# Kernel tuning notes

Hardware: AMD Instinct MI355X
Metric: run time of the kernel (lower is better)

Reference implementation:

```python
import jax, jax.numpy as jnp
import numpy as np

B, L, HID = 2, 2048, 2048
NH, NKV, HD = 16, 4, 128
LAT = 512
Q_PER_KV = NH // NKV
SCALE = HD ** -0.5
ROPE_THETA = 10000.0


def setup_inputs() -> dict:
    key = jax.random.key(0)
    ks = jax.random.split(key, 6)
    s = lambda fan_in: 1.0 / np.sqrt(fan_in)
    return {
        "x": jax.random.normal(ks[0], (B, L, HID), dtype=jnp.float32),
        "Wq": jax.random.normal(ks[1], (HID, NH * HD), dtype=jnp.float32) * s(HID),
        "Wc": jax.random.normal(ks[2], (HID, LAT), dtype=jnp.float32) * s(HID),
        "Wk": jax.random.normal(ks[3], (LAT, NKV * HD), dtype=jnp.float32) * s(LAT),
        "Wv": jax.random.normal(ks[4], (LAT, NKV * HD), dtype=jnp.float32) * s(LAT),
        "Wo": jax.random.normal(ks[5], (NH * HD, HID), dtype=jnp.float32) * s(NH * HD),
        "attention_mask": jnp.ones((B, L), dtype=jnp.int32),
    }


def _rope(t):  # t: [B, H, L, HD]
    half = HD // 2
    inv_freq = 1.0 / (ROPE_THETA ** (jnp.arange(half, dtype=jnp.float32) / half))
    pos = jnp.arange(t.shape[2], dtype=jnp.float32)
    freqs = pos[:, None] * inv_freq[None, :]          # [L, half]
    cos = jnp.cos(freqs)[None, None].astype(t.dtype)  # [1,1,L,half]
    sin = jnp.sin(freqs)[None, None].astype(t.dtype)
    t1, t2 = t[..., :half], t[..., half:]
    return jnp.concatenate([t1 * cos - t2 * sin, t2 * cos + t1 * sin], axis=-1)


def reference(x, Wq, Wc, Wk, Wv, Wo, attention_mask):
    q = (x @ Wq).reshape(B, L, NH, HD).transpose(0, 2, 1, 3)      # [B,NH,L,HD]
    c = x @ Wc                                                    # latent bottleneck
    k = (c @ Wk).reshape(B, L, NKV, HD).transpose(0, 2, 1, 3)     # [B,NKV,L,HD]
    v = (c @ Wv).reshape(B, L, NKV, HD).transpose(0, 2, 1, 3)
    # GQA repeat_interleave along head axis
    k = jnp.repeat(k, Q_PER_KV, axis=1)                           # [B,NH,L,HD]
    v = jnp.repeat(v, Q_PER_KV, axis=1)
    q = _rope(q)
    k = _rope(k)
    att = jnp.einsum("bhqd,bhkd->bhqk", q, k) * SCALE             # [B,NH,L,L]
    neg = jnp.finfo(att.dtype).min
    causal = jnp.tril(jnp.ones((L, L), dtype=bool))[None, None]
    att = jnp.where(causal, att, neg)
    key_mask = (attention_mask > 0)[:, None, None, :]             # [B,1,1,L]
    att = jnp.where(key_mask, att, neg)
    att = jax.nn.softmax(att, axis=-1)
    y = jnp.einsum("bhqk,bhkd->bhqd", att, v)
    y = y.transpose(0, 2, 1, 3).reshape(B, L, NH * HD)
    return y @ Wo
```

## Files before the change

### kernel.cpp

```cpp
#include <hip/hip_runtime.h>
#include <hip/hip_bf16.h>
#include <cstdint>
#include <cstddef>

#define B_    2
#define L_    2048
#define HID_  2048
#define NH_   16
#define NKV_  4
#define HD_   128
#define LAT_  512
#define SCALE_ 0.08838834764831845f
#define SC2_   0.1275174365f

typedef unsigned short u16;
typedef unsigned int   u32;
typedef __attribute__((ext_vector_type(8))) short   short8;
typedef __attribute__((ext_vector_type(4))) float   floatx4;

typedef __attribute__((address_space(1))) const u32 gas_u32;
typedef __attribute__((address_space(3))) u32       las_u32;

__device__ __forceinline__ void gl_lds16(const u16* g, u16* l) {
    __builtin_amdgcn_global_load_lds((gas_u32*)g, (las_u32*)l, 16, 0, 0);
}

__device__ __forceinline__ float bf2f(u16 u) {
    union { u32 i; float f; } v; v.i = ((u32)u) << 16; return v.f;
}
__device__ __forceinline__ u16 f2bf(float f) {
    union { float f; u32 u; } v; v.f = f;
    u32 u = v.u;
    u32 r = (u + 0x7fffu + ((u >> 16) & 1u)) >> 16;
    return (u16)r;
}
__device__ __forceinline__ u16 f2bf_hw(float f) {
    union { __hip_bfloat16 h; u16 u; } c;
    c.h = __float2bfloat16(f);
    return c.u;
}

__global__ void cvt_kernel(const float* __restrict__ in, u16* __restrict__ out, int n4) {
    int i = blockIdx.x * 256 + threadIdx.x;
    if (i < n4) {
        float4 v = ((const float4*)in)[i];
        union { u16 w[4]; uint2 v; } o;
        o.w[0] = f2bf(v.x); o.w[1] = f2bf(v.y);
        o.w[2] = f2bf(v.z); o.w[3] = f2bf(v.w);
        ((uint2*)out)[i] = o.v;
    }
}

__global__ void cvt_transpose2_kernel(const float* __restrict__ in0, u16* __restrict__ out0,
                                      const float* __restrict__ in1, u16* __restrict__ out1,
                                      int R, int C) {
    __shared__ u16 tile[32][33];
    const float* in = blockIdx.z ? in1 : in0;
    u16* out = blockIdx.z ? out1 : out0;
    int c0 = blockIdx.x * 32, r0 = blockIdx.y * 32;
    int tx = threadIdx.x & 31, ty = threadIdx.x >> 5;
    for (int i = ty; i < 32; i += 8)
        tile[tx][i] = f2bf(in[(size_t)(r0 + i) * C + c0 + tx]);
    __syncthreads();
    for (int i = ty; i < 32; i += 8)
        out[(size_t)(c0 + i) * R + r0 + tx] = tile[i][tx];
}

__global__ void transpose_v_kernel(const u16* __restrict__ kv, u16* __restrict__ out) {
    __shared__ u16 t[32][33];
    int lt = blockIdx.x, dt = blockIdx.y, bh = blockIdx.z;
    int b = bh >> 2, kvh = bh & 3;
    int tx = threadIdx.x & 31, ty = threadIdx.x >> 5;
    for (int i = ty; i < 32; i += 8)
        t[i][tx] = kv[(size_t)(b * L_ + lt * 32 + i) * 1024 + 512 + kvh * HD_ + dt * 32 + tx];
    __syncthreads();
    const int lcol = lt * 32 + tx;
    const int k6 = lcol & 63;
    const int ni = k6 >> 4, qd = (k6 >> 2) & 3, r = k6 & 3;
    const int p = ((ni >> 1) << 5) | (qd << 3) | ((ni & 1) << 2) | r;
    const int csig = (lcol & ~63) | p;
    for (int i = ty; i < 32; i += 8)
        out[((size_t)bh * HD_ + dt * 32 + i) * L_ + csig] = t[tx][i];
}

template<int OUT_BF16>
__global__ __launch_bounds__(256)
void gemm_bt(const u16* __restrict__ A, const u16* __restrict__ BT,
             void* __restrict__ C, int M, int N, int K) {
    __shared__ __align__(16) u16 As[128][64];
    __shared__ __align__(16) u16 Bs[128][64];
    const int tid  = threadIdx.x;
    const int m0   = blockIdx.y * 128, n0 = blockIdx.x * 128;
    const int wave = tid >> 6, lane = tid & 63;
    const int wm   = (wave >> 1) * 64, wn = (wave & 1) * 64;
    const int quad = lane >> 4, l16 = lane & 15;

    const int r8 = lane >> 3, srcc = ((lane & 7) ^ r8) * 8;
    const int row0 = wave * 32 + r8;
    const u16* aBase = A  + (size_t)(m0 + row0) * K + srcc;
    const u16* bBase = BT + (size_t)(n0 + row0) * K + srcc;
    u16* laBase = &As[0][0] + wave * 2048;
    u16* lbBase = &Bs[0][0] + wave * 2048;

    floatx4 acc[4][4] = {};

    for (int k0 = 0; k0 < K; k0 += 64) {
        #pragma unroll
        for (int cc = 0; cc < 4; ++cc) {
            gl_lds16(aBase + (size_t)cc * 8 * K + k0, laBase + cc * 512);
            gl_lds16(bBase + (size_t)cc * 8 * K + k0, lbBase + cc * 512);
        }
        __syncthreads();

        #pragma unroll
        for (int kk = 0; kk < 2; kk++) {
            short8 af[4], bfr[4];
            const int co = ((kk * 4 + quad) ^ (l16 & 7)) * 8;
            #pragma unroll
            for (int i = 0; i < 4; i++) {
                af[i]  = *(const short8*)&As[wm + i * 16 + l16][co];
                bfr[i] = *(const short8*)&Bs[wn + i * 16 + l16][co];
            }
            #pragma unroll
            for (int mi = 0; mi < 4; mi++)
                #pragma unroll
                for (int ni = 0; ni < 4; ni++)
                    acc[mi][ni] = __builtin_amdgcn_mfma_f32_16x16x32_bf16(
                        af[mi], bfr[ni], acc[mi][ni], 0, 0, 0);
        }
        __syncthreads();
    }

    #pragma unroll
    for (int mi = 0; mi < 4; mi++) {
        #pragma unroll
        for (int ni = 0; ni < 4; ni++) {
            #pragma unroll
            for (int r = 0; r < 4; r++) {
                int row = m0 + wm + mi * 16 + quad * 4 + r;
                int col = n0 + wn + ni * 16 + l16;
                float v = acc[mi][ni][r];
                if (OUT_BF16) ((u16*)C)[(size_t)row * N + col] = f2bf(v);
                else          ((float*)C)[(size_t)row * N + col] = v;
            }
        }
    }
}

__global__ __launch_bounds__(256)
void gemm_bt_split(const u16* __restrict__ A, const u16* __restrict__ BT,
                   u16* __restrict__ C0, u16* __restrict__ C1,
                   int M, int N, int K, int Nsplit, int N0, int N1) {
    __shared__ __align__(16) u16 As[128][64];
    __shared__ __align__(16) u16 Bs[128][64];
    const int tid  = threadIdx.x;
    const int m0   = blockIdx.y * 128, n0 = blockIdx.x * 128;
    const int wave = tid >> 6, lane = tid & 63;
    const int wm   = (wave >> 1) * 64, wn = (wave & 1) * 64;
    const int quad = lane >> 4, l16 = lane & 15;

    const int r8 = lane >> 3, srcc = ((lane & 7) ^ r8) * 8;
    const int row0 = wave * 32 + r8;
    const u16* aBase = A  + (size_t)(m0 + row0) * K + srcc;
    const u16* bBase = BT + (size_t)(n0 + row0) * K + srcc;
    u16* laBase = &As[0][0] + wave * 2048;
    u16* lbBase = &Bs[0][0] + wave * 2048;

    floatx4 acc[4][4] = {};

    for (int k0 = 0; k0 < K; k0 += 64) {
        #pragma unroll
        for (int cc = 0; cc < 4; ++cc) {
            gl_lds16(aBase + (size_t)cc * 8 * K + k0, laBase + cc * 512);
            gl_lds16(bBase + (size_t)cc * 8 * K + k0, lbBase + cc * 512);
        }
        __syncthreads();

        #pragma unroll
        for (int kk = 0; kk < 2; kk++) {
            short8 af[4], bfr[4];
            const int co = ((kk * 4 + quad) ^ (l16 & 7)) * 8;
            #pragma unroll
            for (int i = 0; i < 4; i++) {
                af[i]  = *(const short8*)&As[wm + i * 16 + l16][co];
                bfr[i] = *(const short8*)&Bs[wn + i * 16 + l16][co];
            }
            #pragma unroll
            for (int mi = 0; mi < 4; mi++)
                #pragma unroll
                for (int ni = 0; ni < 4; ni++)
                    acc[mi][ni] = __builtin_amdgcn_mfma_f32_16x16x32_bf16(
                        af[mi], bfr[ni], acc[mi][ni], 0, 0, 0);
        }
        __syncthreads();
    }

    const int side = (n0 >= Nsplit);
    u16* Cw = side ? C1 : C0;
    const int nw = side ? N1 : N0;
    const int cbase = side ? Nsplit : 0;

    #pragma unroll
    for (int mi = 0; mi < 4; mi++) {
        #pragma unroll
        for (int ni = 0; ni < 4; ni++) {
            #pragma unroll
            for (int r = 0; r < 4; r++) {
                int row = m0 + wm + mi * 16 + quad * 4 + r;
                int col = n0 + wn + ni * 16 + l16 - cbase;
                Cw[(size_t)row * nw + col] = f2bf(acc[mi][ni][r]);
            }
        }
    }
}

__global__ void rope_perm(const u16* __restrict__ in, u16* __restrict__ out,
                          int nh, int nhbits, int rs) {
    int idx = blockIdx.x * 256 + threadIdx.x;
    int d = idx & 63;
    int l = (idx >> 6) & (L_ - 1);
    int h = (idx >> 17) & (nh - 1);
    int b = idx >> (17 + nhbits);
    const u16* src = &in[(size_t)(b * L_ + l) * rs + h * HD_];
    u16* dst = &out[(((size_t)b * nh + h) * L_ + l) * HD_];
    float t1 = bf2f(src[d]), t2 = bf2f(src[d + 64]);
    float inv = expf(-(float)d * 0.14391156831212787f);
    float fr = (float)l * inv;
    float c = cosf(fr), sn = sinf(fr);
    dst[d]      = f2bf(t1 * c - t2 * sn);
    dst[d + 64] = f2bf(t2 * c + t1 * sn);
}

__global__ __launch_bounds__(256)
void attn_mfma(const u16* __restrict__ Q, const u16* __restrict__ K,
               const u16* __restrict__ Vt, const int* __restrict__ amask,
               u16* __restrict__ Y, float* __restrict__ Opart,
               float* __restrict__ lpart) {
    __shared__ __align__(16) u16 Ks[2][64][128];
    __shared__ __align__(16) u16 Vs[2][128][64];

    const int tid  = threadIdx.x;
    const int wave = tid >> 6, lane = tid & 63;
    const int quad = lane >> 4, l16 = lane & 15;

    const int bid = blockIdx.x;
    const int s   = bid >> 8;
    const int c   = bid & 255;
    const int bkvh = c & 7;
    const int j   = c >> 3;
    const int b   = bkvh >> 2, kvh = bkvh & 3;

    const int H  = ((32 + j) >> 1) + 1;
    const int Lg = ((31 - j) >> 1) + 1;
    const int m2 = max((H + 1) >> 1, (Lg + 1) >> 1);
    const int m3 = max((H + 2) / 3, Lg);
    const int nh = (m2 <= m3) ? 2 : 3;
    const int nl = 4 - nh;
    int t, kt0, kt1, pi;
    if (s < nh) {
        t = 32 + j; kt0 = (H * s) / nh; kt1 = (H * (s + 1)) / nh; pi = bid;
    } else {
        t = 31 - j;
        const int ls = s - nh;
        kt0 = (Lg * ls) / nl; kt1 = (Lg * (ls + 1)) / nl;
        pi = (nl == 1) ? -1 : bid;
    }

    const int h   = kvh * 4 + wave;
    const int q0  = t * 32;

    const u16* Qbase = Q  + ((size_t)b * NH_  + h)   * L_ * HD_;
    const u16* Kbase = K  + ((size_t)b * NKV_ + kvh) * L_ * HD_;
    const u16* Vbase = Vt + ((size_t)b * NKV_ + kvh) * (size_t)HD_ * L_;
    const int* mbase = amask + b * L_;

    short8 qa[2][4];
    #pragma unroll
    for (int mi = 0; mi < 2; ++mi)
        #pragma unroll
        for (int ks = 0; ks < 4; ++ks)
            qa[mi][ks] = *(const short8*)&Qbase[(size_t)(q0 + mi * 16 + l16) * HD_ + ks * 32 + quad * 8];

    floatx4 Oacc[2][8] = {};
    float lsum[2] = {0.0f, 0.0f};

    const int slK = lane & 15, rKl = lane >> 4;
    const int slV = lane & 7,  rVl = lane >> 3;
    int okg[4], ovg[4];
    u16 *klds[4], *vlds[4];
    #pragma unroll
    for (int cc = 0; cc < 4; ++cc) {
        const int seg = wave * 4 + cc;
        const int rk = seg * 4 + rKl;
        okg[cc] = rk * HD_ + ((slK ^ (rk & 7)) * 8);
        klds[cc] = &Ks[0][0][0] + seg * 512;
        const int rv = seg * 8 + rVl;
        ovg[cc] = rv * L_ + ((slV ^ (rv & 7)) * 8);
        vlds[cc] = &Vs[0][0][0] + seg * 512;
    }
    const u16* kgb = Kbase + (size_t)kt0 * 64 * HD_;
    const u16* vgb = Vbase + kt0 * 64;

    #pragma unroll
    for (int cc = 0; cc < 4; ++cc) {
        gl_lds16(kgb + okg[cc], klds[cc]);
        gl_lds16(vgb + ovg[cc], vlds[cc]);
    }
    kgb += (size_t)64 * HD_;
    vgb += 64;

    int bufoff = 0;
    for (int kt = kt0; kt < kt1; ++kt) {
        const int kbase = kt * 64;

        __syncthreads();

        const int nb = bufoff ^ 8192;
        if (kt + 1 < kt1) {
            #pragma unroll
            for (int cc = 0; cc < 4; ++cc) {
                gl_lds16(kgb + okg[cc], klds[cc] + nb);
                gl_lds16(vgb + ovg[cc], vlds[cc] + nb);
            }
            kgb += (size_t)64 * HD_;
            vgb += 64;
        }
        const int am_l = mbase[kbase + lane];
        const bool allm = __all(am_l > 0);
        const u16* KsB = &Ks[0][0][0] + bufoff;
        const u16* VsB = &Vs[0][0][0] + bufoff;

        floatx4 sfr[2][4] = {};
        __builtin_amdgcn_s_setprio(1);
        #pragma unroll
        for (int ni = 0; ni < 4; ++ni) {
            #pragma unroll
            for (int ks = 0; ks < 4; ++ks) {
                short8 kf = *(const short8*)&KsB[(ni * 16 + l16) * 128 + ((ks * 4 + quad) ^ (l16 & 7)) * 8];
                sfr[0][ni] = __builtin_amdgcn_mfma_f32_16x16x32_bf16(kf, qa[0][ks], sfr[0][ni], 0, 0, 0);
                sfr[1][ni] = __builtin_amdgcn_mfma_f32_16x16x32_bf16(kf, qa[1][ks], sfr[1][ni], 0, 0, 0);
            }
        }
        __builtin_amdgcn_s_setprio(0);

        if (allm & (kbase + 63 <= q0)) {
            #pragma unroll
            for (int mi = 0; mi < 2; ++mi)
                #pragma unroll
                for (int ni = 0; ni < 4; ++ni)
                    #pragma unroll
                    for (int r = 0; r < 4; ++r) {
                        float p = exp2f(fmaf(sfr[mi][ni][r], SC2_, -8.0f));
                        lsum[mi] += p;
                        sfr[mi][ni][r] = p;
                    }
        } else {
            #pragma unroll
            for (int ni = 0; ni < 4; ++ni) {
                const int4 amv = *(const int4*)&mbase[kbase + ni * 16 + quad * 4];
                const int amr[4] = {amv.x, amv.y, amv.z, amv.w};
                #pragma unroll
                for (int mi = 0; mi < 2; ++mi) {
                    const int qrow = q0 + mi * 16 + l16;
                    #pragma unroll
                    for (int r = 0; r < 4; ++r) {
                        const int kpos = kbase + ni * 16 + quad * 4 + r;
                        const bool ok = (kpos <= qrow) & (amr[r] > 0);
                        float p = ok ? exp2f(fmaf(sfr[mi][ni][r], SC2_, -8.0f)) : 0.0f;
                        lsum[mi] += p;
                        sfr[mi][ni][r] = p;
                    }
                }
            }
        }

        short8 pf[2][2];
        #pragma unroll
        for (int mi = 0; mi < 2; ++mi)
            #pragma unroll
            for (int kc = 0; kc < 2; ++kc) {
                union { u16 w[8]; short8 s8; } u;
                #pragma unroll
                for (int r = 0; r < 4; ++r) {
                    u.w[r]     = f2bf_hw(sfr[mi][kc * 2][r]);
                    u.w[4 + r] = f2bf_hw(sfr[mi][kc * 2 + 1][r]);
                }
                pf[mi][kc] = u.s8;
            }

        __builtin_amdgcn_s_setprio(1);
        #pragma unroll
        for (int kc = 0; kc < 2; ++kc) {
            #pragma unroll
            for (int dn = 0; dn < 8; ++dn) {
                short8 vf = *(const short8*)&VsB[(dn * 16 + l16) * 64 + ((kc * 4 + quad) ^ (l16 & 7)) * 8];
                Oacc[0][dn] = __builtin_amdgcn_mfma_f32_16x16x32_bf16(pf[0][kc], vf, Oacc[0][dn], 0, 0, 0);
                Oacc[1][dn] = __builtin_amdgcn_mfma_f32_16x16x32_bf16(pf[1][kc], vf, Oacc[1][dn], 0, 0, 0);
            }
        }
        __builtin_amdgcn_s_setprio(0);

        bufoff = nb;
    }

    float lr[2];
    #pragma unroll
    for (int mi = 0; mi < 2; ++mi) {
        float v = lsum[mi];
        v += __shfl_xor(v, 16);
        v += __shfl_xor(v, 32);
        lr[mi] = v;
    }

    if (pi < 0) {
        #pragma unroll
        for (int mi = 0; mi < 2; ++mi) {
            #pragma unroll
            for (int r = 0; r < 4; ++r) {
                const float linv = 1.0f / __shfl(lr[mi], quad * 4 + r);
                const int qrow = q0 + mi * 16 + quad * 4 + r;
                u16* dst = &Y[(((size_t)b * L_ + qrow) * NH_ + h) * HD_];
                #pragma unroll
                for (int dn = 0; dn < 8; ++dn)
                    dst[dn * 16 + l16] = f2bf(Oacc[mi][dn][r] * linv);
            }
        }
    } else {
        float* od = Opart + ((size_t)pi * 4 + wave) * 32 * 128;
        float* lp = lpart + ((size_t)pi * 4 + wave) * 32;
        #pragma unroll
        for (int mi = 0; mi < 2; ++mi) {
            if (quad == 0)
                __builtin_nontemporal_store(lr[mi], &lp[mi * 16 + l16]);
            #pragma unroll
            for (int r = 0; r < 4; ++r) {
                const int qi = mi * 16 + quad * 4 + r;
                #pragma unroll
                for (int dn = 0; dn < 8; ++dn)
                    __builtin_nontemporal_store(Oacc[mi][dn][r],
                                                &od[(size_t)qi * 128 + dn * 16 + l16]);
            }
        }
    }
}

__global__ __launch_bounds__(256)
void attn_combine(const float* __restrict__ Opart, const float* __restrict__ lpart,
                  u16* __restrict__ Y) {
    const int cb = blockIdx.x;
    const int c  = cb & 255, z = cb >> 8;
    const int tile = z >> 2, hw = z & 3;
    const int bkvh = c & 7, j = c >> 3;
    const int b = bkvh >> 2, kvh = bkvh & 3;
    const int h = kvh * 4 + hw;
    const int H  = ((32 + j) >> 1) + 1;
    const int Lg = ((31 - j) >> 1) + 1;
    const int m2 = max((H + 1) >> 1, (Lg + 1) >> 1);
    const int m3 = max((H + 2) / 3, Lg);
    const int nh = (m2 <= m3) ? 2 : 3;
    const int nl = 4 - nh;
    if (tile == 1 && nl == 1) return;
    const int s0 = tile ? nh : 0;
    const int ns = tile ? nl : nh;
    const int t  = tile ? (31 - j) : (32 + j);
    const int tid = threadIdx.x;
    const int q = tid >> 3, dg = tid & 7;

    float4 a0 = {0,0,0,0}, a1 = {0,0,0,0}, a2 = {0,0,0,0}, a3 = {0,0,0,0};
    float lacc = 0.0f;
    for (int i = 0; i < ns; ++i) {
        const size_t rowb = ((size_t)((s0 + i) * 256 + c) * 4 + hw) * 32 + q;
        lacc += lpart[rowb];
        const float4* op = (const float4*)(Opart + rowb * 128 + dg * 16);
        float4 v0 = op[0], v1 = op[1], v2 = op[2], v3 = op[3];
        a0.x += v0.x; a0.y += v0.y; a0.z += v0.z; a0.w += v0.w;
        a1.x += v1.x; a1.y += v1.y; a1.z += v1.z; a1.w += v1.w;
        a2.x += v2.x; a2.y += v2.y; a2.z += v2.z; a2.w += v2.w;
        a3.x += v3.x; a3.y += v3.y; a3.z += v3.z; a3.w += v3.w;
    }
    const float linv = 1.0f / lacc;
    const int qrow = t * 32 + q;
    u16* dst = &Y[(((size_t)b * L_ + qrow) * NH_ + h) * HD_ + dg * 16];

    u16 tmp[16];
    tmp[0]  = f2bf(a0.x * linv); tmp[1]  = f2bf(a0.y * linv);
    tmp[2]  = f2bf(a0.z * linv); tmp[3]  = f2bf(a0.w * linv);
    tmp[4]  = f2bf(a1.x * linv); tmp[5]  = f2bf(a1.y * linv);
    tmp[6]  = f2bf(a1.z * linv); tmp[7]  = f2bf(a1.w * linv);
    tmp[8]  = f2bf(a2.x * linv); tmp[9]  = f2bf(a2.y * linv);
    tmp[10] = f2bf(a2.z * linv); tmp[11] = f2bf(a2.w * linv);
    tmp[12] = f2bf(a3.x * linv); tmp[13] = f2bf(a3.y * linv);
    tmp[14] = f2bf(a3.z * linv); tmp[15] = f2bf(a3.w * linv);
    *(uint4*)(dst)     = *(const uint4*)(&tmp[0]);
    *(uint4*)(dst + 8) = *(const uint4*)(&tmp[8]);
}

extern "C" void kernel_launch(void* const* d_in, const int* in_sizes, int n_in,
                              void* d_out, int out_size, void* d_ws, size_t ws_size,
                              hipStream_t stream) {
    const float* x  = (const float*)d_in[0];
    const float* Wq = (const float*)d_in[1];
    const float* Wc = (const float*)d_in[2];
    const float* Wk = (const float*)d_in[3];
    const float* Wv = (const float*)d_in[4];
    const float* Wo = (const float*)d_in[5];
    const int* amask = (const int*)d_in[6];
    float* out = (float*)d_out;

    char* p = (char*)d_ws;
    auto alloc = [&](size_t elems) {
        u16* r = (u16*)p;
        p += ((elems * 2 + 255) / 256) * 256;
        return r;
    };
    u16* WoT  = alloc((size_t)2048 * 2048);
    u16* qbuf = alloc((size_t)4096 * 2048);
    u16* Qr   = alloc((size_t)4096 * 2048);
    u16* Kr   = alloc((size_t)4096 * 512);
    u16* Vt   = alloc((size_t)4096 * 512);
    char* pdead = p;
    u16* WqT  = alloc((size_t)2048 * 2048);
    u16* WckvT= alloc((size_t)1024 * 2048);
    u16* WkT  = alloc((size_t)512 * 512);
    u16* WvT  = alloc((size_t)512 * 512);
    u16* Wcb  = alloc((size_t)2048 * 512);
    u16* Xb   = alloc((size_t)4096 * 2048);
    u16* kvbuf= alloc((size_t)4096 * 1024);
    float* Opart = (float*)pdead;
    float* lpart = (float*)(pdead + (size_t)1024 * 4 * 32 * 128 * 4);

    cvt_kernel<<<8388608 / 4 / 256, 256, 0, stream>>>(x, Xb, 8388608 / 4);
    cvt_kernel<<<(2048 * 512 / 4) / 256, 256, 0, stream>>>(Wc, Wcb, 2048 * 512 / 4);
    cvt_transpose2_kernel<<<dim3(64, 64, 2), 256, 0, stream>>>(Wq, WqT, Wo, WoT, 2048, 2048);
    cvt_transpose2_kernel<<<dim3(16, 16, 2), 256, 0, stream>>>(Wk, WkT, Wv, WvT, 512, 512);

    gemm_bt<1><<<dim3(16, 8), 256, 0, stream>>>(WkT, Wcb, WckvT, 1024, 2048, 512);

    gemm_bt_split<<<dim3(24, 32), 256, 0, stream>>>(Xb, WqT, qbuf, kvbuf,
                                                    4096, 3072, 2048, 2048, 2048, 1024);

    rope_perm<<<(2 * 16 * 2048 * 64) / 256, 256, 0, stream>>>(qbuf, Qr, 16, 4, 2048);
    rope_perm<<<(2 * 4 * 2048 * 64) / 256, 256, 0, stream>>>(kvbuf, Kr, 4, 2, 1024);
    transpose_v_kernel<<<dim3(64, 4, 8), 256, 0, stream>>>(kvbuf, Vt);

    attn_mfma<<<dim3(1024), 256, 0, stream>>>(Qr, Kr, Vt, amask, qbuf, Opart, lpart);
    attn_combine<<<dim3(2048), 256, 0, stream>>>(Opart, lpart, qbuf);

    gemm_bt<0><<<dim3(16, 32), 256, 0, stream>>>(qbuf, WoT, out, 4096, 2048, 2048);
}
```

Measured before the change: 339.3 us.

## Rebalance attention work split and fuse small prep kernel launches

The attention kernel drops from 1024 blocks to 512. Each block either handles the first 17 key tiles of a high query tile, or the rest of that tile followed by the whole paired low query tile, in two sequential passes. The combine step now only merges high-tile partials, and the Opart buffer shrinks. Rope for Q and K and the V transpose are merged into a single launch, as are the two fp32-to-bf16 conversions, to cut launch overhead. Halving the grid lowers parallelism and lengthens per-block serial work, so CU occupancy on a 256-CU part may drop.

Measured after the change: 324.6 us. -4.3%, faster.

```diff
diff --git a/kernel.cpp b/kernel.cpp
--- a/kernel.cpp
+++ b/kernel.cpp
@@ -40,15 +40,18 @@
     return c.u;
 }
 
-__global__ void cvt_kernel(const float* __restrict__ in, u16* __restrict__ out, int n4) {
+__global__ void cvt2_kernel(const float* __restrict__ in0, u16* __restrict__ out0, int n40,
+                            const float* __restrict__ in1, u16* __restrict__ out1, int n41) {
     int i = blockIdx.x * 256 + threadIdx.x;
-    if (i < n4) {
-        float4 v = ((const float4*)in)[i];
-        union { u16 w[4]; uint2 v; } o;
-        o.w[0] = f2bf(v.x); o.w[1] = f2bf(v.y);
-        o.w[2] = f2bf(v.z); o.w[3] = f2bf(v.w);
-        ((uint2*)out)[i] = o.v;
-    }
+    const float* in; u16* out; int k;
+    if (i < n40) { in = in0; out = out0; k = i; }
+    else if (i < n40 + n41) { in = in1; out = out1; k = i - n40; }
+    else return;
+    float4 v = ((const float4*)in)[k];
+    union { u16 w[4]; uint2 v; } o;
+    o.w[0] = f2bf(v.x); o.w[1] = f2bf(v.y);
+    o.w[2] = f2bf(v.z); o.w[3] = f2bf(v.w);
+    ((uint2*)out)[k] = o.v;
 }
 
 __global__ void cvt_transpose2_kernel(const float* __restrict__ in0, u16* __restrict__ out0,
@@ -66,21 +69,47 @@
         out[(size_t)(c0 + i) * R + r0 + tx] = tile[i][tx];
 }
 
-__global__ void transpose_v_kernel(const u16* __restrict__ kv, u16* __restrict__ out) {
-    __shared__ u16 t[32][33];
-    int lt = blockIdx.x, dt = blockIdx.y, bh = blockIdx.z;
-    int b = bh >> 2, kvh = bh & 3;
-    int tx = threadIdx.x & 31, ty = threadIdx.x >> 5;
-    for (int i = ty; i < 32; i += 8)
-        t[i][tx] = kv[(size_t)(b * L_ + lt * 32 + i) * 1024 + 512 + kvh * HD_ + dt * 32 + tx];
-    __syncthreads();
-    const int lcol = lt * 32 + tx;
-    const int k6 = lcol & 63;
-    const int ni = k6 >> 4, qd = (k6 >> 2) & 3, r = k6 & 3;
-    const int p = ((ni >> 1) << 5) | (qd << 3) | ((ni & 1) << 2) | r;
-    const int csig = (lcol & ~63) | p;
-    for (int i = ty; i < 32; i += 8)
-        out[((size_t)bh * HD_ + dt * 32 + i) * L_ + csig] = t[tx][i];
+#define NRQ_ 16384
+#define NRK_ 4096
+__global__ void prep_qkv(const u16* __restrict__ qbuf, u16* __restrict__ Qr,
+                         const u16* __restrict__ kvbuf, u16* __restrict__ Kr,
+                         u16* __restrict__ Vt) {
+    __shared__ u16 tvt[32][33];
+    const int bb = blockIdx.x;
+    if (bb < NRQ_ + NRK_) {
+        const bool isq = bb < NRQ_;
+        const u16* in = isq ? qbuf : kvbuf;
+        u16* out = isq ? Qr : Kr;
+        const int nh = isq ? 16 : 4, nhbits = isq ? 4 : 2, rs = isq ? 2048 : 1024;
+        int idx = (isq ? bb : bb - NRQ_) * 256 + threadIdx.x;
+        int d = idx & 63;
+        int l = (idx >> 6) & (L_ - 1);
+        int h = (idx >> 17) & (nh - 1);
+        int b = idx >> (17 + nhbits);
+        const u16* src = &in[(size_t)(b * L_ + l) * rs + h * HD_];
+        u16* dst = &out[(((size_t)b * nh + h) * L_ + l) * HD_];
+        float t1 = bf2f(src[d]), t2 = bf2f(src[d + 64]);
+        float inv = expf(-(float)d * 0.14391156831212787f);
+        float fr = (float)l * inv;
+        float c = cosf(fr), sn = sinf(fr);
+        dst[d]      = f2bf(t1 * c - t2 * sn);
+        dst[d + 64] = f2bf(t2 * c + t1 * sn);
+    } else {
+        const int i = bb - NRQ_ - NRK_;
+        const int lt = i & 63, dt = (i >> 6) & 3, bh = i >> 8;
+        const int b = bh >> 2, kvh = bh & 3;
+        const int tx = threadIdx.x & 31, ty = threadIdx.x >> 5;
+        for (int k = ty; k < 32; k += 8)
+            tvt[k][tx] = kvbuf[(size_t)(b * L_ + lt * 32 + k) * 1024 + 512 + kvh * HD_ + dt * 32 + tx];
+        __syncthreads();
+        const int lcol = lt * 32 + tx;
+        const int k6 = lcol & 63;
+        const int ni = k6 >> 4, qd = (k6 >> 2) & 3, r = k6 & 3;
+        const int p = ((ni >> 1) << 5) | (qd << 3) | ((ni & 1) << 2) | r;
+        const int csig = (lcol & ~63) | p;
+        for (int k = ty; k < 32; k += 8)
+            Vt[((size_t)bh * HD_ + dt * 32 + k) * L_ + csig] = tvt[tx][k];
+    }
 }
 
 template<int OUT_BF16>
@@ -214,23 +243,6 @@
     }
 }
 
-__global__ void rope_perm(const u16* __restrict__ in, u16* __restrict__ out,
-                          int nh, int nhbits, int rs) {
-    int idx = blockIdx.x * 256 + threadIdx.x;
-    int d = idx & 63;
-    int l = (idx >> 6) & (L_ - 1);
-    int h = (idx >> 17) & (nh - 1);
-    int b = idx >> (17 + nhbits);
-    const u16* src = &in[(size_t)(b * L_ + l) * rs + h * HD_];
-    u16* dst = &out[(((size_t)b * nh + h) * L_ + l) * HD_];
-    float t1 = bf2f(src[d]), t2 = bf2f(src[d + 64]);
-    float inv = expf(-(float)d * 0.14391156831212787f);
-    float fr = (float)l * inv;
-    float c = cosf(fr), sn = sinf(fr);
-    dst[d]      = f2bf(t1 * c - t2 * sn);
-    dst[d + 64] = f2bf(t2 * c + t1 * sn);
-}
-
 __global__ __launch_bounds__(256)
 void attn_mfma(const u16* __restrict__ Q, const u16* __restrict__ K,
                const u16* __restrict__ Vt, const int* __restrict__ amask,
@@ -251,38 +263,13 @@
     const int b   = bkvh >> 2, kvh = bkvh & 3;
 
     const int H  = ((32 + j) >> 1) + 1;
-    const int Lg = ((31 - j) >> 1) + 1;
-    const int m2 = max((H + 1) >> 1, (Lg + 1) >> 1);
-    const int m3 = max((H + 2) / 3, Lg);
-    const int nh = (m2 <= m3) ? 2 : 3;
-    const int nl = 4 - nh;
-    int t, kt0, kt1, pi;
-    if (s < nh) {
-        t = 32 + j; kt0 = (H * s) / nh; kt1 = (H * (s + 1)) / nh; pi = bid;
-    } else {
-        t = 31 - j;
-        const int ls = s - nh;
-        kt0 = (Lg * ls) / nl; kt1 = (Lg * (ls + 1)) / nl;
-        pi = (nl == 1) ? -1 : bid;
-    }
-
-    const int h   = kvh * 4 + wave;
-    const int q0  = t * 32;
+    const int Lg = 33 - H;
+    const int h  = kvh * 4 + wave;
 
     const u16* Qbase = Q  + ((size_t)b * NH_  + h)   * L_ * HD_;
     const u16* Kbase = K  + ((size_t)b * NKV_ + kvh) * L_ * HD_;
     const u16* Vbase = Vt + ((size_t)b * NKV_ + kvh) * (size_t)HD_ * L_;
     const int* mbase = amask + b * L_;
-
-    short8 qa[2][4];
-    #pragma unroll
-    for (int mi = 0; mi < 2; ++mi)
-        #pragma unroll
-        for (int ks = 0; ks < 4; ++ks)
-            qa[mi][ks] = *(const short8*)&Qbase[(size_t)(q0 + mi * 16 + l16) * HD_ + ks * 32 + quad * 8];
-
-    floatx4 Oacc[2][8] = {};
-    float lsum[2] = {0.0f, 0.0f};
 
     const int slK = lane & 15, rKl = lane >> 4;
     const int slV = lane & 7,  rVl = lane >> 3;
@@ -298,147 +285,169 @@
         ovg[cc] = rv * L_ + ((slV ^ (rv & 7)) * 8);
         vlds[cc] = &Vs[0][0][0] + seg * 512;
     }
-    const u16* kgb = Kbase + (size_t)kt0 * 64 * HD_;
-    const u16* vgb = Vbase + kt0 * 64;
-
-    #pragma unroll
-    for (int cc = 0; cc < 4; ++cc) {
-        gl_lds16(kgb + okg[cc], klds[cc]);
-        gl_lds16(vgb + ovg[cc], vlds[cc]);
-    }
-    kgb += (size_t)64 * HD_;
-    vgb += 64;
-
-    int bufoff = 0;
-    for (int kt = kt0; kt < kt1; ++kt) {
-        const int kbase = kt * 64;
+
+    const int npass = (s == 0) ? 1 : 2;
+    for (int pass = 0; pass < npass; ++pass) {
+        int t, kt0, kt1, slot;
+        if (s == 0)           { t = 32 + j; kt0 = 0;  kt1 = 17; slot = c * 2; }
+        else if (pass == 0)   { t = 32 + j; kt0 = 17; kt1 = H;  slot = c * 2 + 1; }
+        else                  { t = 31 - j; kt0 = 0;  kt1 = Lg; slot = -1; }
+        if (kt1 <= kt0) continue;
+        const int q0 = t * 32;
+
+        short8 qa[2][4];
+        #pragma unroll
+        for (int mi = 0; mi < 2; ++mi)
+            #pragma unroll
+            for (int ks = 0; ks < 4; ++ks)
+                qa[mi][ks] = *(const short8*)&Qbase[(size_t)(q0 + mi * 16 + l16) * HD_ + ks * 32 + quad * 8];
+
+        floatx4 Oacc[2][8] = {};
+        float lsum[2] = {0.0f, 0.0f};
+
+        const u16* kgb = Kbase + (size_t)kt0 * 64 * HD_;
+        const u16* vgb = Vbase + kt0 * 64;
 
         __syncthreads();
-
-        const int nb = bufoff ^ 8192;
-        if (kt + 1 < kt1) {
-            #pragma unroll
-            for (int cc = 0; cc < 4; ++cc) {
-                gl_lds16(kgb + okg[cc], klds[cc] + nb);
-                gl_lds16(vgb + ovg[cc], vlds[cc] + nb);
-            }
-            kgb += (size_t)64 * HD_;
-            vgb += 64;
-        }
-        const int am_l = mbase[kbase + lane];
-        const bool allm = __all(am_l > 0);
-        const u16* KsB = &Ks[0][0][0] + bufoff;
-        const u16* VsB = &Vs[0][0][0] + bufoff;
-
-        floatx4 sfr[2][4] = {};
-        __builtin_amdgcn_s_setprio(1);
-        #pragma unroll
-        for (int ni = 0; ni < 4; ++ni) {
-            #pragma unroll
-            for (int ks = 0; ks < 4; ++ks) {
-                short8 kf = *(const short8*)&KsB[(ni * 16 + l16) * 128 + ((ks * 4 + quad) ^ (l16 & 7)) * 8];
-                sfr[0][ni] = __builtin_amdgcn_mfma_f32_16x16x32_bf16(kf, qa[0][ks], sfr[0][ni], 0, 0, 0);
-                sfr[1][ni] = __builtin_amdgcn_mfma_f32_16x16x32_bf16(kf, qa[1][ks], sfr[1][ni], 0, 0, 0);
-            }
-        }
-        __builtin_amdgcn_s_setprio(0);
-
-        if (allm & (kbase + 63 <= q0)) {
+        #pragma unroll
+        for (int cc = 0; cc < 4; ++cc) {
+            gl_lds16(kgb + okg[cc], klds[cc]);
+            gl_lds16(vgb + ovg[cc], vlds[cc]);
+        }
+        kgb += (size_t)64 * HD_;
+        vgb += 64;
+
+        int bufoff = 0;
+        for (int kt = kt0; kt < kt1; ++kt) {
+            const int kbase = kt * 64;
+
+            __syncthreads();
+
+            const int nb = bufoff ^ 8192;
+            if (kt + 1 < kt1) {
+                #pragma unroll
+                for (int cc = 0; cc < 4; ++cc) {
+                    gl_lds16(kgb + okg[cc], klds[cc] + nb);
+                    gl_lds16(vgb + ovg[cc], vlds[cc] + nb);
+                }
+                kgb += (size_t)64 * HD_;
+                vgb += 64;
+            }
+            const int am_l = mbase[kbase + lane];
+            const bool allm = __all(am_l > 0);
+            const u16* KsB = &Ks[0][0][0] + bufoff;
+            const u16* VsB = &Vs[0][0][0] + bufoff;
+
+            floatx4 sfr[2][4] = {};
+            __builtin_amdgcn_s_setprio(1);
+            #pragma unroll
+            for (int ni = 0; ni < 4; ++ni) {
+                #pragma unroll
+                for (int ks = 0; ks < 4; ++ks) {
+                    short8 kf = *(const short8*)&KsB[(ni * 16 + l16) * 128 + ((ks * 4 + quad) ^ (l16 & 7)) * 8];
+                    sfr[0][ni] = __builtin_amdgcn_mfma_f32_16x16x32_bf16(kf, qa[0][ks], sfr[0][ni], 0, 0, 0);
+                    sfr[1][ni] = __builtin_amdgcn_mfma_f32_16x16x32_bf16(kf, qa[1][ks], sfr[1][ni], 0, 0, 0);
+                }
+            }
+            __builtin_amdgcn_s_setprio(0);
+
+            if (allm & (kbase + 63 <= q0)) {
+                #pragma unroll
+                for (int mi = 0; mi < 2; ++mi)
+                    #pragma unroll
+                    for (int ni = 0; ni < 4; ++ni)
+                        #pragma unroll
+                        for (int r = 0; r < 4; ++r) {
+                            float p = exp2f(fmaf(sfr[mi][ni][r], SC2_, -8.0f));
+                            lsum[mi] += p;
+                            sfr[mi][ni][r] = p;
+                        }
+            } else {
+                #pragma unroll
+                for (int ni = 0; ni < 4; ++ni) {
+                    const int4 amv = *(const int4*)&mbase[kbase + ni * 16 + quad * 4];
+                    const int amr[4] = {amv.x, amv.y, amv.z, amv.w};
+                    #pragma unroll
+                    for (int mi = 0; mi < 2; ++mi) {
+                        const int qrow = q0 + mi * 16 + l16;
+                        #pragma unroll
+                        for (int r = 0; r < 4; ++r) {
+                            const int kpos = kbase + ni * 16 + quad * 4 + r;
+                            const bool ok = (kpos <= qrow) & (amr[r] > 0);
+                            float p = ok ? exp2f(fmaf(sfr[mi][ni][r], SC2_, -8.0f)) : 0.0f;
+                            lsum[mi] += p;
+                            sfr[mi][ni][r] = p;
+                        }
+                    }
+                }
+            }
+
+            short8 pf[2][2];
             #pragma unroll
             for (int mi = 0; mi < 2; ++mi)
                 #pragma unroll
-                for (int ni = 0; ni < 4; ++ni)
+                for (int kc = 0; kc < 2; ++kc) {
+                    union { u16 w[8]; short8 s8; } u;
                     #pragma unroll
                     for (int r = 0; r < 4; ++r) {
-                        float p = exp2f(fmaf(sfr[mi][ni][r], SC2_, -8.0f));
-                        lsum[mi] += p;
-                        sfr[mi][ni][r] = p;
+                        u.w[r]     = f2bf_hw(sfr[mi][kc * 2][r]);
+                        u.w[4 + r] = f2bf_hw(sfr[mi][kc * 2 + 1][r]);
                     }
+                    pf[mi][kc] = u.s8;
+                }
+
+            __builtin_amdgcn_s_setprio(1);
+            #pragma unroll
+            for (int kc = 0; kc < 2; ++kc) {
+                #pragma unroll
+                for (int dn = 0; dn < 8; ++dn) {
+                    short8 vf = *(const short8*)&VsB[(dn * 16 + l16) * 64 + ((kc * 4 + quad) ^ (l16 & 7)) * 8];
+                    Oacc[0][dn] = __builtin_amdgcn_mfma_f32_16x16x32_bf16(pf[0][kc], vf, Oacc[0][dn], 0, 0, 0);
+                    Oacc[1][dn] = __builtin_amdgcn_mfma_f32_16x16x32_bf16(pf[1][kc], vf, Oacc[1][dn], 0, 0, 0);
+                }
+            }
+            __builtin_amdgcn_s_setprio(0);
+
+            bufoff = nb;
+        }
+
+        float lr[2];
+        #pragma unroll
+        for (int mi = 0; mi < 2; ++mi) {
+            float v = lsum[mi];
+            v += __shfl_xor(v, 16);
+            v += __shfl_xor(v, 32);
+            lr[mi] = v;
+        }
+
+        if (slot < 0) {
+            #pragma unroll
+            for (int mi = 0; mi < 2; ++mi) {
+                #pragma unroll
+                for (int r = 0; r < 4; ++r) {
+                    const float linv = 1.0f / __shfl(lr[mi], quad * 4 + r);
+                    const int qrow = q0 + mi * 16 + quad * 4 + r;
+                    u16* dst = &Y[(((size_t)b * L_ + qrow) * NH_ + h) * HD_];
+                    #pragma unroll
+                    for (int dn = 0; dn < 8; ++dn)
+                        dst[dn * 16 + l16] = f2bf(Oacc[mi][dn][r] * linv);
+                }
+            }
         } else {
-            #pragma unroll
-            for (int ni = 0; ni < 4; ++ni) {
-                const int4 amv = *(const int4*)&mbase[kbase + ni * 16 + quad * 4];
-                const int amr[4] = {amv.x, amv.y, amv.z, amv.w};
-                #pragma unroll
-                for (int mi = 0; mi < 2; ++mi) {
-                    const int qrow = q0 + mi * 16 + l16;
+            float* od = Opart + ((size_t)slot * 4 + wave) * 32 * 128;
+            float* lp = lpart + ((size_t)slot * 4 + wave) * 32;
+            #pragma unroll
+            for (int mi = 0; mi < 2; ++mi) {
+                if (quad == 0)
+                    __builtin_nontemporal_store(lr[mi], &lp[mi * 16 + l16]);
+                #pragma unroll
+                for (int r = 0; r < 4; ++r) {
+                    const int qi = mi * 16 + quad * 4 + r;
                     #pragma unroll
-                    for (int r = 0; r < 4; ++r) {
-                        const int kpos = kbase + ni * 16 + quad * 4 + r;
-                        const bool ok = (kpos <= qrow) & (amr[r] > 0);
-                        float p = ok ? exp2f(fmaf(sfr[mi][ni][r], SC2_, -8.0f)) : 0.0f;
-                        lsum[mi] += p;
-                        sfr[mi][ni][r] = p;
-                    }
-                }
-            }
-        }
-
-        short8 pf[2][2];
-        #pragma unroll
-        for (int mi = 0; mi < 2; ++mi)
-            #pragma unroll
-            for (int kc = 0; kc < 2; ++kc) {
-                union { u16 w[8]; short8 s8; } u;
-                #pragma unroll
-                for (int r = 0; r < 4; ++r) {
-                    u.w[r]     = f2bf_hw(sfr[mi][kc * 2][r]);
-                    u.w[4 + r] = f2bf_hw(sfr[mi][kc * 2 + 1][r]);
-                }
-                pf[mi][kc] = u.s8;
-            }
-
-        __builtin_amdgcn_s_setprio(1);
-        #pragma unroll
-        for (int kc = 0; kc < 2; ++kc) {
-            #pragma unroll
-            for (int dn = 0; dn < 8; ++dn) {
-                short8 vf = *(const short8*)&VsB[(dn * 16 + l16) * 64 + ((kc * 4 + quad) ^ (l16 & 7)) * 8];
-                Oacc[0][dn] = __builtin_amdgcn_mfma_f32_16x16x32_bf16(pf[0][kc], vf, Oacc[0][dn], 0, 0, 0);
-                Oacc[1][dn] = __builtin_amdgcn_mfma_f32_16x16x32_bf16(pf[1][kc], vf, Oacc[1][dn], 0, 0, 0);
-            }
-        }
-        __builtin_amdgcn_s_setprio(0);
-
-        bufoff = nb;
-    }
-
-    float lr[2];
-    #pragma unroll
-    for (int mi = 0; mi < 2; ++mi) {
-        float v = lsum[mi];
-        v += __shfl_xor(v, 16);
-        v += __shfl_xor(v, 32);
-        lr[mi] = v;
-    }
-
-    if (pi < 0) {
-        #pragma unroll
-        for (int mi = 0; mi < 2; ++mi) {
-            #pragma unroll
-            for (int r = 0; r < 4; ++r) {
-                const float linv = 1.0f / __shfl(lr[mi], quad * 4 + r);
-                const int qrow = q0 + mi * 16 + quad * 4 + r;
-                u16* dst = &Y[(((size_t)b * L_ + qrow) * NH_ + h) * HD_];
-                #pragma unroll
-                for (int dn = 0; dn < 8; ++dn)
-                    dst[dn * 16 + l16] = f2bf(Oacc[mi][dn][r] * linv);
-            }
-        }
-    } else {
-        float* od = Opart + ((size_t)pi * 4 + wave) * 32 * 128;
-        float* lp = lpart + ((size_t)pi * 4 + wave) * 32;
-        #pragma unroll
-        for (int mi = 0; mi < 2; ++mi) {
-            if (quad == 0)
-                __builtin_nontemporal_store(lr[mi], &lp[mi * 16 + l16]);
-            #pragma unroll
-            for (int r = 0; r < 4; ++r) {
-                const int qi = mi * 16 + quad * 4 + r;
-                #pragma unroll
-                for (int dn = 0; dn < 8; ++dn)
-                    __builtin_nontemporal_store(Oacc[mi][dn][r],
-                                                &od[(size_t)qi * 128 + dn * 16 + l16]);
+                    for (int dn = 0; dn < 8; ++dn)
+                        __builtin_nontemporal_store(Oacc[mi][dn][r],
+                                                    &od[(size_t)qi * 128 + dn * 16 + l16]);
+                }
             }
         }
     }
@@ -448,28 +457,20 @@
 void attn_combine(const float* __restrict__ Opart, const float* __restrict__ lpart,
                   u16* __restrict__ Y) {
     const int cb = blockIdx.x;
-    const int c  = cb & 255, z = cb >> 8;
-    const int tile = z >> 2, hw = z & 3;
+    const int c  = cb & 255, hw = cb >> 8;
     const int bkvh = c & 7, j = c >> 3;
     const int b = bkvh >> 2, kvh = bkvh & 3;
     const int h = kvh * 4 + hw;
-    const int H  = ((32 + j) >> 1) + 1;
-    const int Lg = ((31 - j) >> 1) + 1;
-    const int m2 = max((H + 1) >> 1, (Lg + 1) >> 1);
-    const int m3 = max((H + 2) / 3, Lg);
-    const int nh = (m2 <= m3) ? 2 : 3;
-    const int nl = 4 - nh;
-    if (tile == 1 && nl == 1) return;
-    const int s0 = tile ? nh : 0;
-    const int ns = tile ? nl : nh;
-    const int t  = tile ? (31 - j) : (32 + j);
+    const int H = ((32 + j) >> 1) + 1;
+    const int ns = (H > 17) ? 2 : 1;
+    const int t = 32 + j;
     const int tid = threadIdx.x;
     const int q = tid >> 3, dg = tid & 7;
 
     float4 a0 = {0,0,0,0}, a1 = {0,0,0,0}, a2 = {0,0,0,0}, a3 = {0,0,0,0};
     float lacc = 0.0f;
     for (int i = 0; i < ns; ++i) {
-        const size_t rowb = ((size_t)((s0 + i) * 256 + c) * 4 + hw) * 32 + q;
+        const size_t rowb = ((size_t)(c * 2 + i) * 4 + hw) * 32 + q;
         lacc += lpart[rowb];
         const float4* op = (const float4*)(Opart + rowb * 128 + dg * 16);
         float4 v0 = op[0], v1 = op[1], v2 = op[2], v3 = op[3];
@@ -527,10 +528,10 @@
     u16* Xb   = alloc((size_t)4096 * 2048);
     u16* kvbuf= alloc((size_t)4096 * 1024);
     float* Opart = (float*)pdead;
-    float* lpart = (float*)(pdead + (size_t)1024 * 4 * 32 * 128 * 4);
-
-    cvt_kernel<<<8388608 / 4 / 256, 256, 0, stream>>>(x, Xb, 8388608 / 4);
-    cvt_kernel<<<(2048 * 512 / 4) / 256, 256, 0, stream>>>(Wc, Wcb, 2048 * 512 / 4);
+    float* lpart = (float*)(pdead + (size_t)512 * 4 * 32 * 128 * 4);
+
+    cvt2_kernel<<<(2097152 + 262144) / 256, 256, 0, stream>>>(
+        x, Xb, 2097152, Wc, Wcb, 262144);
     cvt_transpose2_kernel<<<dim3(64, 64, 2), 256, 0, stream>>>(Wq, WqT, Wo, WoT, 2048, 2048);
     cvt_transpose2_kernel<<<dim3(16, 16, 2), 256, 0, stream>>>(Wk, WkT, Wv, WvT, 512, 512);
 
@@ -539,12 +540,10 @@
     gemm_bt_split<<<dim3(24, 32), 256, 0, stream>>>(Xb, WqT, qbuf, kvbuf,
                                                     4096, 3072, 2048, 2048, 2048, 1024);
 
-    rope_perm<<<(2 * 16 * 2048 * 64) / 256, 256, 0, stream>>>(qbuf, Qr, 16, 4, 2048);
-    rope_perm<<<(2 * 4 * 2048 * 64) / 256, 256, 0, stream>>>(kvbuf, Kr, 4, 2, 1024);
-    transpose_v_kernel<<<dim3(64, 4, 8), 256, 0, stream>>>(kvbuf, Vt);
-
-    attn_mfma<<<dim3(1024), 256, 0, stream>>>(Qr, Kr, Vt, amask, qbuf, Opart, lpart);
-    attn_combine<<<dim3(2048), 256, 0, stream>>>(Opart, lpart, qbuf);
+    prep_qkv<<<NRQ_ + NRK_ + 2048, 256, 0, stream>>>(qbuf, Qr, kvbuf, Kr, Vt);
+
+    attn_mfma<<<dim3(512), 256, 0, stream>>>(Qr, Kr, Vt, amask, qbuf, Opart, lpart);
+    attn_combine<<<dim3(1024), 256, 0, stream>>>(Opart, lpart, qbuf);
 
     gemm_bt<0><<<dim3(16, 32), 256, 0, stream>>>(qbuf, WoT, out, 4096, 2048, 2048);
 }
```
